# Performance work log

Measured on AMD Instinct MI355X. Metric: run time of the kernel, lower is better.

The kernel has to match this reference:

```python
import jax, jax.numpy as jnp
import numpy as np

N_HEAD = 16
D_HEAD = 64
D_MODEL = 1024
SCALE = 1.0 / float(D_HEAD) ** 0.5
LN_EPS = 1e-5


def _rel_shift(x):
    # x: [b, n, i, j] -> Transformer-XL relative shift
    b, n, i, j = x.shape
    x = jnp.pad(x, ((0, 0), (0, 0), (0, 0), (1, 0)))  # zero-pad front of last dim
    x = x.reshape(b, n, j + 1, i)[:, :, 1:, :]
    return x.reshape(b, n, i, j)


def _layer_norm(x, g, b):
    mu = jnp.mean(x, axis=-1, keepdims=True)
    var = jnp.mean(jnp.square(x - mu), axis=-1, keepdims=True)
    return g * (x - mu) / jnp.sqrt(var + LN_EPS) + b


def setup_inputs() -> dict:
    key = jax.random.key(0)
    ks = jax.random.split(key, 8)
    qlen, bsz = 1024, 4
    w = jax.random.normal(ks[0], (qlen, bsz, D_MODEL), jnp.float32)
    r = jax.random.normal(ks[1], (qlen, D_MODEL), jnp.float32)
    r_w_bias = 0.02 * jax.random.normal(ks[2], (N_HEAD, D_HEAD), jnp.float32)
    r_r_bias = 0.02 * jax.random.normal(ks[3], (N_HEAD, D_HEAD), jnp.float32)
    attn_mask = jnp.triu(jnp.ones((qlen, qlen), bool), 1)  # causal, True = masked
    qkv_w = 0.02 * jax.random.normal(ks[4], (D_MODEL, 3 * N_HEAD * D_HEAD), jnp.float32)
    qkv_b = jnp.zeros((3 * N_HEAD * D_HEAD,), jnp.float32)
    rk_w = 0.02 * jax.random.normal(ks[5], (D_MODEL, N_HEAD * D_HEAD), jnp.float32)
    rk_b = jnp.zeros((N_HEAD * D_HEAD,), jnp.float32)
    o_w = 0.02 * jax.random.normal(ks[6], (N_HEAD * D_HEAD, D_MODEL), jnp.float32)
    o_b = jnp.zeros((D_MODEL,), jnp.float32)
    ln_g = jnp.ones((D_MODEL,), jnp.float32)
    ln_b = jnp.zeros((D_MODEL,), jnp.float32)
    return {"w": w, "r": r, "r_w_bias": r_w_bias, "r_r_bias": r_r_bias,
            "qkv_w": qkv_w, "qkv_b": qkv_b, "rk_w": rk_w, "rk_b": rk_b,
            "o_w": o_w, "o_b": o_b, "ln_g": ln_g, "ln_b": ln_b,
            "attn_mask": attn_mask}


def reference(w, r, r_w_bias, r_r_bias, qkv_w, qkv_b, rk_w, rk_b, o_w, o_b, ln_g, ln_b, attn_mask):
    qlen, bsz, _ = w.shape
    # post-lnorm path (pre_lnorm=False)
    heads = w @ qkv_w + qkv_b                       # [q, b, 3*H*D]
    q, k, v = jnp.split(heads, 3, axis=-1)
    q = q.reshape(qlen, bsz, N_HEAD, D_HEAD)
    k = k.reshape(qlen, bsz, N_HEAD, D_HEAD)
    v = v.reshape(qlen, bsz, N_HEAD, D_HEAD)
    rk = (r @ rk_w + rk_b).reshape(-1, N_HEAD, D_HEAD)  # [rlen, H, D]
    AC = jnp.einsum('ibnd,jbnd->bnij', q + r_w_bias, k)
    BD = _rel_shift(jnp.einsum('ibnd,jnd->bnij', q + r_r_bias, rk))
    score = SCALE * (AC + BD)                       # [b, H, q, k]
    score = jnp.where(attn_mask[None, None, :, :], -jnp.inf, score)
    prob = jax.nn.softmax(score, axis=-1)
    vec = jnp.einsum('bnij,jbnd->ibnd', prob, v).reshape(qlen, bsz, N_HEAD * D_HEAD)
    attn_out = vec @ o_w + o_b
    return _layer_norm(w + attn_out, ln_g, ln_b)
```

## Files before the change

kernel.cpp:

```cpp
#include <hip/hip_runtime.h>
#include <math.h>

#define QL 1024
#define BSZ 4
#define NH 16
#define DH 64
#define DM 1024
#define SCALE_F 0.125f

typedef __attribute__((ext_vector_type(8))) short bf16x8;
typedef __attribute__((ext_vector_type(4))) float f32x4;

__device__ __forceinline__ unsigned short f2bf(float f) {
  union { float f; unsigned int u; } c; c.f = f;
  unsigned int u = c.u;
  u += 0x7FFFu + ((u >> 16) & 1u);
  return (unsigned short)(u >> 16);
}
__device__ __forceinline__ float bf2f(unsigned short u) {
  union { unsigned int i; float f; } c; c.i = ((unsigned int)u) << 16;
  return c.f;
}
__device__ __forceinline__ float2 bfp2f(const unsigned short* p) {
  unsigned int u = *(const unsigned int*)p;
  union { unsigned int u; float f; } lo, hi;
  lo.u = (u & 0xFFFFu) << 16;
  hi.u = u & 0xFFFF0000u;
  return make_float2(lo.f, hi.f);
}

__device__ __forceinline__ void ld_lds16(const unsigned short* g, unsigned short* l) {
  __builtin_amdgcn_global_load_lds(
      (const __attribute__((address_space(1))) unsigned int*)g,
      (__attribute__((address_space(3))) unsigned int*)l, 16, 0, 0);
}

__device__ __forceinline__ bf16x8 frag64(const unsigned short* lds, int n, int s) {
  return *(const bf16x8*)(lds + n * 64 + ((s ^ (n & 7)) * 8));
}

__global__ __launch_bounds__(256) void prep_kernel(
    const float* __restrict__ w, const float* __restrict__ r,
    const float* __restrict__ qkv_w, const float* __restrict__ rk_w,
    const float* __restrict__ o_w,
    unsigned short* __restrict__ wb, unsigned short* __restrict__ rb,
    unsigned short* __restrict__ qkv_wt, unsigned short* __restrict__ rk_wt,
    unsigned short* __restrict__ o_wt) {
  __shared__ __align__(16) unsigned short t[64][72];
  const int bid = blockIdx.x, tid = threadIdx.x;
  if (bid < 2560) {
    const float* in = (bid < 2048) ? w : r;
    unsigned short* out = (bid < 2048) ? wb : rb;
    int idx = ((bid < 2048) ? bid : (bid - 2048)) * 256 + tid;
    float4 a = *(const float4*)(in + (size_t)idx * 8);
    float4 b = *(const float4*)(in + (size_t)idx * 8 + 4);
    unsigned short o[8] = {f2bf(a.x), f2bf(a.y), f2bf(a.z), f2bf(a.w),
                           f2bf(b.x), f2bf(b.y), f2bf(b.z), f2bf(b.w)};
    *(uint4*)(out + (size_t)idx * 8) = *(const uint4*)o;
    return;
  }
  const float* in; unsigned short* out; int N, n0, k0;
  if (bid < 3328) {
    int l = bid - 2560; in = qkv_w; out = qkv_wt; N = 3072;
    n0 = (l % 48) * 64; k0 = (l / 48) * 64;
  } else if (bid < 3584) {
    int l = bid - 3328; in = rk_w; out = rk_wt; N = 1024;
    n0 = (l & 15) * 64; k0 = (l >> 4) * 64;
  } else {
    int l = bid - 3584; in = o_w; out = o_wt; N = 1024;
    n0 = (l & 15) * 64; k0 = (l >> 4) * 64;
  }
  for (int f = tid; f < 1024; f += 256) {
    int rr = f >> 4, c4 = (f & 15) * 4;
    float4 v = *(const float4*)(in + (size_t)(k0 + rr) * N + n0 + c4);
    t[c4 + 0][rr] = f2bf(v.x); t[c4 + 1][rr] = f2bf(v.y);
    t[c4 + 2][rr] = f2bf(v.z); t[c4 + 3][rr] = f2bf(v.w);
  }
  __syncthreads();
  for (int f = tid; f < 512; f += 256) {
    int rr = f >> 3, seg = (f & 7) * 8;
    *(uint4*)(out + (size_t)(n0 + rr) * 1024 + k0 + seg) = *(const uint4*)&t[rr][seg];
  }
}

__global__ __launch_bounds__(256) void drk_kernel(const unsigned short* __restrict__ rkb,
                                                  const float* __restrict__ rwb,
                                                  const float* __restrict__ rrb,
                                                  float* __restrict__ drk) {
  int idx = blockIdx.x * 256 + threadIdx.x;
  int h = idx >> 10;
  const unsigned short* rp = rkb + (size_t)idx * DH;
  float s = 0.f;
  for (int d = 0; d < DH; d += 2) {
    float2 rv = bfp2f(rp + d);
    s += rv.x * (rrb[h * DH + d] - rwb[h * DH + d]) +
         rv.y * (rrb[h * DH + d + 1] - rwb[h * DH + d + 1]);
  }
  drk[idx] = s;
}

template <int MODE>
__global__ __launch_bounds__(256) void gemm_bt(
    const unsigned short* __restrict__ A, const unsigned short* __restrict__ BT,
    const float* __restrict__ bias, float* __restrict__ Cf,
    unsigned short* __restrict__ O0, unsigned short* __restrict__ O1,
    unsigned short* __restrict__ O2, int M, int N, int K) {
  __shared__ __align__(16) unsigned short As[2 * 128 * 32];
  __shared__ __align__(16) unsigned short Bs[2 * 128 * 32];
  const int tid = threadIdx.x;
  const int w = tid >> 6, lane = tid & 63;
  const int quad = lane >> 4, l15 = lane & 15;
  const int wr = w >> 1, wc = w & 1;
  const int bm = blockIdx.y * 128, bn = blockIdx.x * 128;
  const int r_ = lane >> 2, sg = lane & 3;
  const int gs = sg ^ (r_ & 3);
  f32x4 acc[4][4] = {};

  auto stage = [&](int bf, int k0) {
#pragma unroll
    for (int i = 0; i < 2; ++i) {
      int row = (w * 2 + i) * 16 + r_;
      ld_lds16(A + (size_t)(bm + row) * K + k0 + gs * 8, As + bf * 4096 + (w * 2 + i) * 512);
      ld_lds16(BT + (size_t)(bn + row) * K + k0 + gs * 8, Bs + bf * 4096 + (w * 2 + i) * 512);
    }
  };

  int buf = 0;
  stage(0, 0);
  for (int k0 = 0; k0 < K; k0 += 32) {
    __syncthreads();
    if (k0 + 32 < K) stage(buf ^ 1, k0 + 32);
    const unsigned short* Al = As + buf * 4096;
    const unsigned short* Bl = Bs + buf * 4096;
    const int sa = quad ^ (l15 & 3);
    bf16x8 af[4], bf[4];
#pragma unroll
    for (int rt = 0; rt < 4; ++rt)
      af[rt] = *(const bf16x8*)&Al[(wr * 64 + rt * 16 + l15) * 32 + sa * 8];
#pragma unroll
    for (int nt = 0; nt < 4; ++nt)
      bf[nt] = *(const bf16x8*)&Bl[(wc * 64 + nt * 16 + l15) * 32 + sa * 8];
#pragma unroll
    for (int rt = 0; rt < 4; ++rt)
#pragma unroll
      for (int nt = 0; nt < 4; ++nt)
        acc[rt][nt] = __builtin_amdgcn_mfma_f32_16x16x32_bf16(af[rt], bf[nt], acc[rt][nt], 0, 0, 0);
    buf ^= 1;
  }

#pragma unroll
  for (int rt = 0; rt < 4; ++rt)
#pragma unroll
    for (int nt = 0; nt < 4; ++nt) {
      int gc = bn + wc * 64 + nt * 16 + l15;
      float bv = bias[gc];
#pragma unroll
      for (int reg = 0; reg < 4; ++reg) {
        int gr = bm + wr * 64 + rt * 16 + quad * 4 + reg;
        float val = acc[rt][nt][reg] + bv;
        if (MODE == 0) {
          int part = gc >> 10, h = (gc >> 6) & 15, d = gc & 63;
          int i = gr >> 2, b = gr & 3;
          if (part == 0)
            O0[((size_t)((b * NH + h) * QL + i)) * DH + d] = f2bf(val);
          else if (part == 1)
            O1[((size_t)((b * NH + h) * QL + i)) * DH + d] = f2bf(val);
          else
            O2[((size_t)((b * NH + h) * DH + d)) * QL + i] = f2bf(val);
        } else if (MODE == 1) {
          int h = gc >> 6, d = gc & 63;
          O0[((size_t)(h * QL + gr)) * DH + d] = f2bf(val);
        } else {
          Cf[(size_t)gr * N + gc] = val;
        }
      }
    }
}

__global__ __launch_bounds__(256, 4) void attn_kernel(
    const unsigned short* __restrict__ qbf, const unsigned short* __restrict__ kbf,
    const unsigned short* __restrict__ vtb, const unsigned short* __restrict__ rkb,
    const float* __restrict__ drk, const float* __restrict__ rwb,
    unsigned short* __restrict__ vecb) {
  __shared__ __align__(16) unsigned short ks[2 * 4096];
  __shared__ __align__(16) unsigned short vt[2 * 4096];
  __shared__ __align__(16) unsigned short bandps[4096];

  const int tid = threadIdx.x;
  const int w = tid >> 6, lane = tid & 63;
  const int quad = lane >> 4, l15 = lane & 15;
  const int bh = blockIdx.x, b = bh >> 4, h = bh & 15;
  const int i0 = (15 - (int)blockIdx.y) * 64;
  const int tdiag = i0 >> 6;

  const unsigned short* kB0 = kbf + (size_t)bh * QL * DH;
  const unsigned short* vB0 = vtb + (size_t)bh * DH * QL;
  const unsigned short* rB0 = rkb + (size_t)h * QL * DH;
  const float* drkh = drk + h * QL;

  const int srow = lane >> 3, sseg = lane & 7;

  auto stage_tile = [&](const unsigned short* gbase, size_t rstride, unsigned short* lds) {
#pragma unroll
    for (int ii = 0; ii < 2; ++ii) {
      int r = ii * 32 + w * 8 + srow;
      int gseg = sseg ^ (r & 7);
      ld_lds16(gbase + (size_t)r * rstride + gseg * 8, lds + ii * 2048 + w * 512);
    }
  };

  bf16x8 qf[2];
  {
    int qrow = i0 + w * 16 + l15;
    const unsigned short* qp = qbf + ((size_t)bh * QL + qrow) * DH;
#pragma unroll
    for (int s = 0; s < 2; ++s) {
      int off = s * 32 + quad * 8;
      uint4 raw = *(const uint4*)(qp + off);
      const unsigned short* ru = (const unsigned short*)&raw;
      float4 wb0 = *(const float4*)(rwb + h * DH + off);
      float4 wb1 = *(const float4*)(rwb + h * DH + off + 4);
      union { bf16x8 v; unsigned short u[8]; } qc;
      qc.u[0] = f2bf(bf2f(ru[0]) + wb0.x); qc.u[1] = f2bf(bf2f(ru[1]) + wb0.y);
      qc.u[2] = f2bf(bf2f(ru[2]) + wb0.z); qc.u[3] = f2bf(bf2f(ru[3]) + wb0.w);
      qc.u[4] = f2bf(bf2f(ru[4]) + wb1.x); qc.u[5] = f2bf(bf2f(ru[5]) + wb1.y);
      qc.u[6] = f2bf(bf2f(ru[6]) + wb1.z); qc.u[7] = f2bf(bf2f(ru[7]) + wb1.w);
      qf[s] = qc.v;
    }
  }

  auto rel_frag = [&](int gb, f32x4& c, float& dv) {
    int gc = min(gb + l15, 1023);
    const unsigned short* rp = rB0 + (size_t)gc * DH;
    f32x4 a = {0.f, 0.f, 0.f, 0.f};
    a = __builtin_amdgcn_mfma_f32_16x16x32_bf16(qf[0], *(const bf16x8*)(rp + quad * 8), a, 0, 0, 0);
    a = __builtin_amdgcn_mfma_f32_16x16x32_bf16(qf[1], *(const bf16x8*)(rp + 32 + quad * 8), a, 0, 0, 0);
    c = a;
    dv = drkh[gc];
  };

  stage_tile(kB0, DH, ks);
  stage_tile(vB0, QL, vt);

  f32x4 racc[5];
  float drkv[5];
#pragma unroll
  for (int i = 0; i < 5; ++i) rel_frag(1008 - i0 - 16 * w + 16 * i, racc[i], drkv[i]);

  float mrow[4], lrow[4];
  f32x4 pv[4];
#pragma unroll
  for (int r = 0; r < 4; ++r) {
    mrow[r] = -1e30f; lrow[r] = 0.f;
    pv[r] = (f32x4){0.f, 0.f, 0.f, 0.f};
  }

  int buf = 0;
  for (int t = 0; t <= tdiag; ++t) {
    __syncthreads();
    if (t < tdiag) {
      int j1 = (t + 1) << 6;
      stage_tile(kB0 + (size_t)j1 * DH, DH, ks + (buf ^ 1) * 4096);
      stage_tile(vB0 + j1, QL, vt + (buf ^ 1) * 4096);
    }
    if (t > 0) {
#pragma unroll
      for (int i = 0; i < 4; ++i) { racc[i] = racc[i + 1]; drkv[i] = drkv[i + 1]; }
#pragma unroll
      for (int i = 1; i < 5; ++i)
        rel_frag(1008 - i0 + 64 * t - 16 * w + 16 * i, racc[i], drkv[i]);
    }
    const int j0 = t << 6;
    const bool diag = (t == tdiag);
    const unsigned short* ksl = ks + buf * 4096;
    const unsigned short* vtl = vt + buf * 4096;

    f32x4 sacc[4];
#pragma unroll
    for (int nt = 0; nt < 4; ++nt) {
      int n = nt * 16 + l15;
      f32x4 c = {0.f, 0.f, 0.f, 0.f};
      c = __builtin_amdgcn_mfma_f32_16x16x32_bf16(qf[0], frag64(ksl, n, quad), c, 0, 0, 0);
      c = __builtin_amdgcn_mfma_f32_16x16x32_bf16(qf[1], frag64(ksl, n, 4 + quad), c, 0, 0, 0);
      sacc[nt] = c;
    }

#pragma unroll
    for (int i = 0; i < 5; ++i) {
      float dv = drkv[i];
#pragma unroll
      for (int r = 0; r < 4; ++r) {
        int c = 16 * i + l15 + 4 * quad + r - 15;
        int il = w * 16 + quad * 4 + r;
        if (c >= 0 && c < 64)
          bandps[il * 64 + (c ^ ((il & 7) << 3))] = f2bf(racc[i][r] + dv);
      }
    }

#pragma unroll
    for (int r = 0; r < 4; ++r) {
      const int il = w * 16 + quad * 4 + r;
      const int sw = (il & 7) << 3;
      float sv[4], smax = -1e30f;
#pragma unroll
      for (int nt = 0; nt < 4; ++nt) {
        int jl = nt * 16 + l15;
        float s = (sacc[nt][r] + bf2f(bandps[il * 64 + (jl ^ sw)])) * SCALE_F;
        if (diag && jl > il) s = -1e30f;
        sv[nt] = s;
        smax = fmaxf(smax, s);
      }
      smax = fmaxf(smax, __shfl_xor(smax, 1));
      smax = fmaxf(smax, __shfl_xor(smax, 2));
      smax = fmaxf(smax, __shfl_xor(smax, 4));
      smax = fmaxf(smax, __shfl_xor(smax, 8));
      float mnew = fmaxf(mrow[r], smax);
      float alpha = __expf(mrow[r] - mnew);
      mrow[r] = mnew;
      float psum = 0.f;
#pragma unroll
      for (int nt = 0; nt < 4; ++nt) {
        float e = __expf(sv[nt] - mnew);
        bandps[il * 64 + ((nt * 16 + l15) ^ sw)] = f2bf(e);
        psum += e;
      }
      psum += __shfl_xor(psum, 1);
      psum += __shfl_xor(psum, 2);
      psum += __shfl_xor(psum, 4);
      psum += __shfl_xor(psum, 8);
      lrow[r] = lrow[r] * alpha + psum;
#pragma unroll
      for (int nt = 0; nt < 4; ++nt) pv[nt][r] *= alpha;
    }

    {
      const int ilr = w * 16 + l15;
      const int swr = ilr & 7;
      bf16x8 pf0 = *(const bf16x8*)&bandps[ilr * 64 + ((quad ^ swr) * 8)];
      bf16x8 pf1 = *(const bf16x8*)&bandps[ilr * 64 + (((4 + quad) ^ swr) * 8)];
#pragma unroll
      for (int nt = 0; nt < 4; ++nt) {
        int n = nt * 16 + l15;
        pv[nt] = __builtin_amdgcn_mfma_f32_16x16x32_bf16(pf0, frag64(vtl, n, quad), pv[nt], 0, 0, 0);
        pv[nt] = __builtin_amdgcn_mfma_f32_16x16x32_bf16(pf1, frag64(vtl, n, 4 + quad), pv[nt], 0, 0, 0);
      }
    }
    buf ^= 1;
  }

#pragma unroll
  for (int nt = 0; nt < 4; ++nt)
#pragma unroll
    for (int reg = 0; reg < 4; ++reg) {
      int il = w * 16 + quad * 4 + reg;
      int gi = i0 + il;
      int d = nt * 16 + l15;
      float val = pv[nt][reg] / lrow[reg];
      vecb[((size_t)(gi * BSZ + b)) * DM + h * DH + d] = f2bf(val);
    }
}

__global__ __launch_bounds__(256) void ln_kernel(
    const float* __restrict__ w, const float* __restrict__ attn,
    const float* __restrict__ g, const float* __restrict__ bta,
    float* __restrict__ out) {
  __shared__ float red[4];
  __shared__ float sval[2];
  const int row = blockIdx.x, tid = threadIdx.x;
  const float* wr = w + (size_t)row * DM;
  const float* ar = attn + (size_t)row * DM;
  float4 wv = *(const float4*)(wr + tid * 4);
  float4 av = *(const float4*)(ar + tid * 4);
  float x0 = wv.x + av.x, x1 = wv.y + av.y, x2 = wv.z + av.z, x3 = wv.w + av.w;
  float s = x0 + x1 + x2 + x3;
#pragma unroll
  for (int off = 32; off; off >>= 1) s += __shfl_down(s, off, 64);
  const int lane = tid & 63, wvi = tid >> 6;
  if (lane == 0) red[wvi] = s;
  __syncthreads();
  if (tid == 0) sval[0] = (red[0] + red[1] + red[2] + red[3]) * (1.0f / 1024.0f);
  __syncthreads();
  const float mu = sval[0];
  float d0 = x0 - mu, d1 = x1 - mu, d2 = x2 - mu, d3 = x3 - mu;
  float vs2 = d0 * d0 + d1 * d1 + d2 * d2 + d3 * d3;
#pragma unroll
  for (int off = 32; off; off >>= 1) vs2 += __shfl_down(vs2, off, 64);
  if (lane == 0) red[wvi] = vs2;
  __syncthreads();
  if (tid == 0)
    sval[1] = rsqrtf((red[0] + red[1] + red[2] + red[3]) * (1.0f / 1024.0f) + 1e-5f);
  __syncthreads();
  const float inv = sval[1];
  float4 gv = *(const float4*)(g + tid * 4);
  float4 bv = *(const float4*)(bta + tid * 4);
  float4 ov;
  ov.x = gv.x * d0 * inv + bv.x;
  ov.y = gv.y * d1 * inv + bv.y;
  ov.z = gv.z * d2 * inv + bv.z;
  ov.w = gv.w * d3 * inv + bv.w;
  *(float4*)(out + (size_t)row * DM + tid * 4) = ov;
}

extern "C" void kernel_launch(void* const* d_in, const int* in_sizes, int n_in,
                              void* d_out, int out_size, void* d_ws, size_t ws_size,
                              hipStream_t stream) {
  const float* w     = (const float*)d_in[0];
  const float* r     = (const float*)d_in[1];
  const float* rwb   = (const float*)d_in[2];
  const float* rrb   = (const float*)d_in[3];
  const float* qkv_w = (const float*)d_in[4];
  const float* qkv_b = (const float*)d_in[5];
  const float* rk_w  = (const float*)d_in[6];
  const float* rk_b  = (const float*)d_in[7];
  const float* o_w   = (const float*)d_in[8];
  const float* o_b   = (const float*)d_in[9];
  const float* ln_g  = (const float*)d_in[10];
  const float* ln_b  = (const float*)d_in[11];

  float* out = (float*)d_out;
  char* p = (char*)d_ws;
  unsigned short* wb     = (unsigned short*)p; p += (size_t)4096 * 1024 * 2;
  unsigned short* rb     = (unsigned short*)p; p += (size_t)1024 * 1024 * 2;
  unsigned short* qkv_wt = (unsigned short*)p; p += (size_t)3072 * 1024 * 2;
  unsigned short* rk_wt  = (unsigned short*)p; p += (size_t)1024 * 1024 * 2;
  unsigned short* o_wt   = (unsigned short*)p; p += (size_t)1024 * 1024 * 2;
  unsigned short* qbf    = (unsigned short*)p; p += (size_t)BSZ * NH * QL * DH * 2;
  unsigned short* kbf    = (unsigned short*)p; p += (size_t)BSZ * NH * QL * DH * 2;
  unsigned short* vtb    = (unsigned short*)p; p += (size_t)BSZ * NH * QL * DH * 2;
  unsigned short* rkbf   = (unsigned short*)p; p += (size_t)NH * QL * DH * 2;
  float*          drk    = (float*)p;          p += (size_t)NH * QL * 4;
  unsigned short* vecb   = (unsigned short*)p; p += (size_t)4096 * 1024 * 2;
  float*          attnf  = (float*)p;          p += (size_t)4096 * 1024 * 4;

  prep_kernel<<<3840, 256, 0, stream>>>(w, r, qkv_w, rk_w, o_w,
                                        wb, rb, qkv_wt, rk_wt, o_wt);
  gemm_bt<0><<<dim3(24, 32), 256, 0, stream>>>(wb, qkv_wt, qkv_b, nullptr,
                                               qbf, kbf, vtb, 4096, 3072, 1024);
  gemm_bt<1><<<dim3(8, 8), 256, 0, stream>>>(rb, rk_wt, rk_b, nullptr,
                                             rkbf, nullptr, nullptr, 1024, 1024, 1024);
  drk_kernel<<<64, 256, 0, stream>>>(rkbf, rwb, rrb, drk);
  attn_kernel<<<dim3(64, 16), 256, 0, stream>>>(qbf, kbf, vtb, rkbf, drk, rwb, vecb);
  gemm_bt<2><<<dim3(8, 32), 256, 0, stream>>>(vecb, o_wt, o_b, attnf,
                                              nullptr, nullptr, nullptr, 4096, 1024, 1024);
  ln_kernel<<<4096, 256, 0, stream>>>(w, attnf, ln_g, ln_b, out);
}
```

Before: 313.2 us.

## Merge QKV and rel-key GEMMs with drk fusion, pair causal attention tiles per block

The QKV and relative-key projections now run in one 832-block, 512-thread GEMM launch. The rel-key epilogue computes drk with shuffle reductions and atomicAdd after a memset, which removes the separate drk kernel. The output GEMM also moves to 512 threads with 4x2 wave tiling. The attention kernel processes two query tiles per block (y and 15-y) so every block does the same amount of causal work, sharing K/V staging across both, and the grid is halved. The cost is more registers per attention thread, with the occupancy hint dropped, plus atomic traffic for drk.

Measured after the change: 307.9 us. About the same (-1.7%).

```diff
diff --git a/kernel.cpp b/kernel.cpp
--- a/kernel.cpp
+++ b/kernel.cpp
@@ -83,115 +83,197 @@
   }
 }
 
-__global__ __launch_bounds__(256) void drk_kernel(const unsigned short* __restrict__ rkb,
-                                                  const float* __restrict__ rwb,
-                                                  const float* __restrict__ rrb,
-                                                  float* __restrict__ drk) {
-  int idx = blockIdx.x * 256 + threadIdx.x;
-  int h = idx >> 10;
-  const unsigned short* rp = rkb + (size_t)idx * DH;
-  float s = 0.f;
-  for (int d = 0; d < DH; d += 2) {
-    float2 rv = bfp2f(rp + d);
-    s += rv.x * (rrb[h * DH + d] - rwb[h * DH + d]) +
-         rv.y * (rrb[h * DH + d + 1] - rwb[h * DH + d + 1]);
-  }
-  drk[idx] = s;
-}
-
-template <int MODE>
-__global__ __launch_bounds__(256) void gemm_bt(
+__global__ __launch_bounds__(512) void gemm12(
+    const unsigned short* __restrict__ wb, const unsigned short* __restrict__ rb,
+    const unsigned short* __restrict__ qkv_wt, const unsigned short* __restrict__ rk_wt,
+    const float* __restrict__ qkv_b, const float* __restrict__ rk_b,
+    const float* __restrict__ rwb, const float* __restrict__ rrb,
+    unsigned short* __restrict__ qbf, unsigned short* __restrict__ kbf,
+    unsigned short* __restrict__ vtb, unsigned short* __restrict__ rkbf,
+    float* __restrict__ drk) {
+  __shared__ __align__(16) unsigned short As[2 * 4096];
+  __shared__ __align__(16) unsigned short Bs[2 * 4096];
+  const int bid = blockIdx.x, tid = threadIdx.x;
+  const int w = tid >> 6, lane = tid & 63;
+  const int quad = lane >> 4, l15 = lane & 15;
+  const int wr = w >> 2, wc = w & 3;
+  const bool job0 = bid < 768;
+  const unsigned short *A, *BT;
+  const float* bias;
+  int bm, bn;
+  if (job0) {
+    A = wb; BT = qkv_wt; bias = qkv_b;
+    bn = (bid % 24) * 128; bm = (bid / 24) * 128;
+  } else {
+    int l = bid - 768;
+    A = rb; BT = rk_wt; bias = rk_b;
+    bn = (l & 7) * 128; bm = (l >> 3) * 128;
+  }
+  const int srow = w * 16 + (lane >> 2);
+  const int sseg = (lane & 3) ^ ((lane >> 2) & 3);
+  f32x4 acc[4][2] = {};
+
+  auto stage = [&](int bf, int k0) {
+    ld_lds16(A + (size_t)(bm + srow) * 1024 + k0 + sseg * 8, As + bf * 4096 + w * 512);
+    ld_lds16(BT + (size_t)(bn + srow) * 1024 + k0 + sseg * 8, Bs + bf * 4096 + w * 512);
+  };
+
+  int buf = 0;
+  stage(0, 0);
+  for (int k0 = 0; k0 < 1024; k0 += 32) {
+    __syncthreads();
+    if (k0 + 32 < 1024) stage(buf ^ 1, k0 + 32);
+    const unsigned short* Al = As + buf * 4096;
+    const unsigned short* Bl = Bs + buf * 4096;
+    const int sa = quad ^ (l15 & 3);
+    bf16x8 af[4], bfr[2];
+#pragma unroll
+    for (int rt = 0; rt < 4; ++rt)
+      af[rt] = *(const bf16x8*)&Al[(wr * 64 + rt * 16 + l15) * 32 + sa * 8];
+#pragma unroll
+    for (int nt = 0; nt < 2; ++nt)
+      bfr[nt] = *(const bf16x8*)&Bl[(wc * 32 + nt * 16 + l15) * 32 + sa * 8];
+#pragma unroll
+    for (int rt = 0; rt < 4; ++rt)
+#pragma unroll
+      for (int nt = 0; nt < 2; ++nt)
+        acc[rt][nt] = __builtin_amdgcn_mfma_f32_16x16x32_bf16(af[rt], bfr[nt], acc[rt][nt], 0, 0, 0);
+    buf ^= 1;
+  }
+
+  if (job0) {
+#pragma unroll
+    for (int rt = 0; rt < 4; ++rt)
+#pragma unroll
+      for (int nt = 0; nt < 2; ++nt) {
+        int gc = bn + wc * 32 + nt * 16 + l15;
+        float bv = bias[gc];
+        int part = gc >> 10, h = (gc >> 6) & 15, d = gc & 63;
+#pragma unroll
+        for (int reg = 0; reg < 4; ++reg) {
+          int gr = bm + wr * 64 + rt * 16 + quad * 4 + reg;
+          float val = acc[rt][nt][reg] + bv;
+          int i = gr >> 2, b = gr & 3;
+          if (part == 0)
+            qbf[((size_t)((b * NH + h) * QL + i)) * DH + d] = f2bf(val);
+          else if (part == 1)
+            kbf[((size_t)((b * NH + h) * QL + i)) * DH + d] = f2bf(val);
+          else
+            vtb[((size_t)((b * NH + h) * DH + d)) * QL + i] = f2bf(val);
+        }
+      }
+  } else {
+    const int h = (bn + wc * 32) >> 6;
+    float df[2];
+#pragma unroll
+    for (int nt = 0; nt < 2; ++nt) {
+      int dd = (wc & 1) * 32 + nt * 16 + l15;
+      df[nt] = rrb[h * DH + dd] - rwb[h * DH + dd];
+    }
+#pragma unroll
+    for (int rt = 0; rt < 4; ++rt) {
+      float s[4] = {0.f, 0.f, 0.f, 0.f};
+#pragma unroll
+      for (int nt = 0; nt < 2; ++nt) {
+        int gc = bn + wc * 32 + nt * 16 + l15;
+        float bv = bias[gc];
+        int d = gc & 63;
+#pragma unroll
+        for (int reg = 0; reg < 4; ++reg) {
+          int gr = bm + wr * 64 + rt * 16 + quad * 4 + reg;
+          float val = acc[rt][nt][reg] + bv;
+          rkbf[((size_t)(h * QL + gr)) * DH + d] = f2bf(val);
+          s[reg] += val * df[nt];
+        }
+      }
+#pragma unroll
+      for (int reg = 0; reg < 4; ++reg) {
+        float v = s[reg];
+        v += __shfl_xor(v, 1);
+        v += __shfl_xor(v, 2);
+        v += __shfl_xor(v, 4);
+        v += __shfl_xor(v, 8);
+        if (l15 == 0) {
+          int j = bm + wr * 64 + rt * 16 + quad * 4 + reg;
+          atomicAdd(&drk[h * QL + j], v);
+        }
+      }
+    }
+  }
+}
+
+__global__ __launch_bounds__(512) void gemm_o(
     const unsigned short* __restrict__ A, const unsigned short* __restrict__ BT,
-    const float* __restrict__ bias, float* __restrict__ Cf,
-    unsigned short* __restrict__ O0, unsigned short* __restrict__ O1,
-    unsigned short* __restrict__ O2, int M, int N, int K) {
-  __shared__ __align__(16) unsigned short As[2 * 128 * 32];
-  __shared__ __align__(16) unsigned short Bs[2 * 128 * 32];
+    const float* __restrict__ bias, float* __restrict__ Cf) {
+  __shared__ __align__(16) unsigned short As[2 * 4096];
+  __shared__ __align__(16) unsigned short Bs[2 * 4096];
   const int tid = threadIdx.x;
   const int w = tid >> 6, lane = tid & 63;
   const int quad = lane >> 4, l15 = lane & 15;
-  const int wr = w >> 1, wc = w & 1;
+  const int wr = w >> 2, wc = w & 3;
   const int bm = blockIdx.y * 128, bn = blockIdx.x * 128;
-  const int r_ = lane >> 2, sg = lane & 3;
-  const int gs = sg ^ (r_ & 3);
-  f32x4 acc[4][4] = {};
+  const int srow = w * 16 + (lane >> 2);
+  const int sseg = (lane & 3) ^ ((lane >> 2) & 3);
+  f32x4 acc[4][2] = {};
 
   auto stage = [&](int bf, int k0) {
-#pragma unroll
-    for (int i = 0; i < 2; ++i) {
-      int row = (w * 2 + i) * 16 + r_;
-      ld_lds16(A + (size_t)(bm + row) * K + k0 + gs * 8, As + bf * 4096 + (w * 2 + i) * 512);
-      ld_lds16(BT + (size_t)(bn + row) * K + k0 + gs * 8, Bs + bf * 4096 + (w * 2 + i) * 512);
-    }
+    ld_lds16(A + (size_t)(bm + srow) * 1024 + k0 + sseg * 8, As + bf * 4096 + w * 512);
+    ld_lds16(BT + (size_t)(bn + srow) * 1024 + k0 + sseg * 8, Bs + bf * 4096 + w * 512);
   };
 
   int buf = 0;
   stage(0, 0);
-  for (int k0 = 0; k0 < K; k0 += 32) {
+  for (int k0 = 0; k0 < 1024; k0 += 32) {
     __syncthreads();
-    if (k0 + 32 < K) stage(buf ^ 1, k0 + 32);
+    if (k0 + 32 < 1024) stage(buf ^ 1, k0 + 32);
     const unsigned short* Al = As + buf * 4096;
     const unsigned short* Bl = Bs + buf * 4096;
     const int sa = quad ^ (l15 & 3);
-    bf16x8 af[4], bf[4];
+    bf16x8 af[4], bfr[2];
 #pragma unroll
     for (int rt = 0; rt < 4; ++rt)
       af[rt] = *(const bf16x8*)&Al[(wr * 64 + rt * 16 + l15) * 32 + sa * 8];
 #pragma unroll
-    for (int nt = 0; nt < 4; ++nt)
-      bf[nt] = *(const bf16x8*)&Bl[(wc * 64 + nt * 16 + l15) * 32 + sa * 8];
+    for (int nt = 0; nt < 2; ++nt)
+      bfr[nt] = *(const bf16x8*)&Bl[(wc * 32 + nt * 16 + l15) * 32 + sa * 8];
 #pragma unroll
     for (int rt = 0; rt < 4; ++rt)
 #pragma unroll
-      for (int nt = 0; nt < 4; ++nt)
-        acc[rt][nt] = __builtin_amdgcn_mfma_f32_16x16x32_bf16(af[rt], bf[nt], acc[rt][nt], 0, 0, 0);
+      for (int nt = 0; nt < 2; ++nt)
+        acc[rt][nt] = __builtin_amdgcn_mfma_f32_16x16x32_bf16(af[rt], bfr[nt], acc[rt][nt], 0, 0, 0);
     buf ^= 1;
   }
 
 #pragma unroll
   for (int rt = 0; rt < 4; ++rt)
 #pragma unroll
-    for (int nt = 0; nt < 4; ++nt) {
-      int gc = bn + wc * 64 + nt * 16 + l15;
+    for (int nt = 0; nt < 2; ++nt) {
+      int gc = bn + wc * 32 + nt * 16 + l15;
       float bv = bias[gc];
 #pragma unroll
       for (int reg = 0; reg < 4; ++reg) {
         int gr = bm + wr * 64 + rt * 16 + quad * 4 + reg;
-        float val = acc[rt][nt][reg] + bv;
-        if (MODE == 0) {
-          int part = gc >> 10, h = (gc >> 6) & 15, d = gc & 63;
-          int i = gr >> 2, b = gr & 3;
-          if (part == 0)
-            O0[((size_t)((b * NH + h) * QL + i)) * DH + d] = f2bf(val);
-          else if (part == 1)
-            O1[((size_t)((b * NH + h) * QL + i)) * DH + d] = f2bf(val);
-          else
-            O2[((size_t)((b * NH + h) * DH + d)) * QL + i] = f2bf(val);
-        } else if (MODE == 1) {
-          int h = gc >> 6, d = gc & 63;
-          O0[((size_t)(h * QL + gr)) * DH + d] = f2bf(val);
-        } else {
-          Cf[(size_t)gr * N + gc] = val;
-        }
-      }
-    }
-}
-
-__global__ __launch_bounds__(256, 4) void attn_kernel(
+        Cf[(size_t)gr * DM + gc] = acc[rt][nt][reg] + bv;
+      }
+    }
+}
+
+__global__ __launch_bounds__(256) void attn_kernel(
     const unsigned short* __restrict__ qbf, const unsigned short* __restrict__ kbf,
     const unsigned short* __restrict__ vtb, const unsigned short* __restrict__ rkb,
     const float* __restrict__ drk, const float* __restrict__ rwb,
     unsigned short* __restrict__ vecb) {
   __shared__ __align__(16) unsigned short ks[2 * 4096];
   __shared__ __align__(16) unsigned short vt[2 * 4096];
-  __shared__ __align__(16) unsigned short bandps[4096];
+  __shared__ __align__(16) unsigned short band[2][4096];
 
   const int tid = threadIdx.x;
   const int w = tid >> 6, lane = tid & 63;
   const int quad = lane >> 4, l15 = lane & 15;
   const int bh = blockIdx.x, b = bh >> 4, h = bh & 15;
-  const int i0 = (15 - (int)blockIdx.y) * 64;
-  const int tdiag = i0 >> 6;
+  const int yA = blockIdx.y;
+  const int i0A = yA * 64, i0B = (15 - yA) * 64;
+  const int tA = yA, tB = 15 - yA;
 
   const unsigned short* kB0 = kbf + (size_t)bh * QL * DH;
   const unsigned short* vB0 = vtb + (size_t)bh * DH * QL;
@@ -199,7 +281,6 @@
   const float* drkh = drk + h * QL;
 
   const int srow = lane >> 3, sseg = lane & 7;
-
   auto stage_tile = [&](const unsigned short* gbase, size_t rstride, unsigned short* lds) {
 #pragma unroll
     for (int ii = 0; ii < 2; ++ii) {
@@ -209,8 +290,7 @@
     }
   };
 
-  bf16x8 qf[2];
-  {
+  auto load_q = [&](int i0, bf16x8* qf) {
     int qrow = i0 + w * 16 + l15;
     const unsigned short* qp = qbf + ((size_t)bh * QL + qrow) * DH;
 #pragma unroll
@@ -227,10 +307,13 @@
       qc.u[6] = f2bf(bf2f(ru[6]) + wb1.z); qc.u[7] = f2bf(bf2f(ru[7]) + wb1.w);
       qf[s] = qc.v;
     }
-  }
-
-  auto rel_frag = [&](int gb, f32x4& c, float& dv) {
-    int gc = min(gb + l15, 1023);
+  };
+  bf16x8 qfA[2], qfB[2];
+  load_q(i0A, qfA);
+  load_q(i0B, qfB);
+
+  auto rel_frag = [&](int gb, const bf16x8* qf, f32x4& c, float& dv) {
+    int gc = min(gb + l15, QL - 1);
     const unsigned short* rp = rB0 + (size_t)gc * DH;
     f32x4 a = {0.f, 0.f, 0.f, 0.f};
     a = __builtin_amdgcn_mfma_f32_16x16x32_bf16(qf[0], *(const bf16x8*)(rp + quad * 8), a, 0, 0, 0);
@@ -242,39 +325,25 @@
   stage_tile(kB0, DH, ks);
   stage_tile(vB0, QL, vt);
 
-  f32x4 racc[5];
-  float drkv[5];
-#pragma unroll
-  for (int i = 0; i < 5; ++i) rel_frag(1008 - i0 - 16 * w + 16 * i, racc[i], drkv[i]);
-
-  float mrow[4], lrow[4];
-  f32x4 pv[4];
+  f32x4 raccA[5], raccB[5];
+  float dvA[5], dvB[5];
+#pragma unroll
+  for (int i = 0; i < 5; ++i) {
+    rel_frag(1008 - i0A - 16 * w + 16 * i, qfA, raccA[i], dvA[i]);
+    rel_frag(1008 - i0B - 16 * w + 16 * i, qfB, raccB[i], dvB[i]);
+  }
+
+  float mA[4], lA[4], mB[4], lB[4];
+  f32x4 pvA[4], pvB[4];
 #pragma unroll
   for (int r = 0; r < 4; ++r) {
-    mrow[r] = -1e30f; lrow[r] = 0.f;
-    pv[r] = (f32x4){0.f, 0.f, 0.f, 0.f};
-  }
-
-  int buf = 0;
-  for (int t = 0; t <= tdiag; ++t) {
-    __syncthreads();
-    if (t < tdiag) {
-      int j1 = (t + 1) << 6;
-      stage_tile(kB0 + (size_t)j1 * DH, DH, ks + (buf ^ 1) * 4096);
-      stage_tile(vB0 + j1, QL, vt + (buf ^ 1) * 4096);
-    }
-    if (t > 0) {
-#pragma unroll
-      for (int i = 0; i < 4; ++i) { racc[i] = racc[i + 1]; drkv[i] = drkv[i + 1]; }
-#pragma unroll
-      for (int i = 1; i < 5; ++i)
-        rel_frag(1008 - i0 + 64 * t - 16 * w + 16 * i, racc[i], drkv[i]);
-    }
-    const int j0 = t << 6;
-    const bool diag = (t == tdiag);
-    const unsigned short* ksl = ks + buf * 4096;
-    const unsigned short* vtl = vt + buf * 4096;
-
+    mA[r] = mB[r] = -1e30f; lA[r] = lB[r] = 0.f;
+    pvA[r] = pvB[r] = (f32x4){0.f, 0.f, 0.f, 0.f};
+  }
+
+  auto do_stream = [&](const bf16x8* qf, f32x4* racc, float* dv, float* mrow, float* lrow,
+                       f32x4* pv, bool diag, const unsigned short* ksl,
+                       const unsigned short* vtl, unsigned short* bandS) {
     f32x4 sacc[4];
 #pragma unroll
     for (int nt = 0; nt < 4; ++nt) {
@@ -284,19 +353,17 @@
       c = __builtin_amdgcn_mfma_f32_16x16x32_bf16(qf[1], frag64(ksl, n, 4 + quad), c, 0, 0, 0);
       sacc[nt] = c;
     }
-
 #pragma unroll
     for (int i = 0; i < 5; ++i) {
-      float dv = drkv[i];
+      float dvv = dv[i];
 #pragma unroll
       for (int r = 0; r < 4; ++r) {
         int c = 16 * i + l15 + 4 * quad + r - 15;
         int il = w * 16 + quad * 4 + r;
         if (c >= 0 && c < 64)
-          bandps[il * 64 + (c ^ ((il & 7) << 3))] = f2bf(racc[i][r] + dv);
-      }
-    }
-
+          bandS[il * 64 + (c ^ ((il & 7) << 3))] = f2bf(racc[i][r] + dvv);
+      }
+    }
 #pragma unroll
     for (int r = 0; r < 4; ++r) {
       const int il = w * 16 + quad * 4 + r;
@@ -305,7 +372,7 @@
 #pragma unroll
       for (int nt = 0; nt < 4; ++nt) {
         int jl = nt * 16 + l15;
-        float s = (sacc[nt][r] + bf2f(bandps[il * 64 + (jl ^ sw)])) * SCALE_F;
+        float s = (sacc[nt][r] + bf2f(bandS[il * 64 + (jl ^ sw)])) * SCALE_F;
         if (diag && jl > il) s = -1e30f;
         sv[nt] = s;
         smax = fmaxf(smax, s);
@@ -321,7 +388,7 @@
 #pragma unroll
       for (int nt = 0; nt < 4; ++nt) {
         float e = __expf(sv[nt] - mnew);
-        bandps[il * 64 + ((nt * 16 + l15) ^ sw)] = f2bf(e);
+        bandS[il * 64 + ((nt * 16 + l15) ^ sw)] = f2bf(e);
         psum += e;
       }
       psum += __shfl_xor(psum, 1);
@@ -332,12 +399,11 @@
 #pragma unroll
       for (int nt = 0; nt < 4; ++nt) pv[nt][r] *= alpha;
     }
-
     {
       const int ilr = w * 16 + l15;
       const int swr = ilr & 7;
-      bf16x8 pf0 = *(const bf16x8*)&bandps[ilr * 64 + ((quad ^ swr) * 8)];
-      bf16x8 pf1 = *(const bf16x8*)&bandps[ilr * 64 + (((4 + quad) ^ swr) * 8)];
+      bf16x8 pf0 = *(const bf16x8*)&bandS[ilr * 64 + ((quad ^ swr) * 8)];
+      bf16x8 pf1 = *(const bf16x8*)&bandS[ilr * 64 + (((4 + quad) ^ swr) * 8)];
 #pragma unroll
       for (int nt = 0; nt < 4; ++nt) {
         int n = nt * 16 + l15;
@@ -345,6 +411,36 @@
         pv[nt] = __builtin_amdgcn_mfma_f32_16x16x32_bf16(pf1, frag64(vtl, n, 4 + quad), pv[nt], 0, 0, 0);
       }
     }
+  };
+
+  int buf = 0;
+  for (int t = 0; t <= tB; ++t) {
+    __syncthreads();
+    if (t < tB) {
+      int j1 = (t + 1) << 6;
+      stage_tile(kB0 + (size_t)j1 * DH, DH, ks + (buf ^ 1) * 4096);
+      stage_tile(vB0 + j1, QL, vt + (buf ^ 1) * 4096);
+    }
+    const unsigned short* ksl = ks + buf * 4096;
+    const unsigned short* vtl = vt + buf * 4096;
+    const bool actA = (t <= tA);
+
+    if (t > 0) {
+      raccB[0] = raccB[4]; dvB[0] = dvB[4];
+      const int GB = 1008 - i0B + 64 * t - 16 * w;
+#pragma unroll
+      for (int i = 1; i < 5; ++i) rel_frag(GB + 16 * i, qfB, raccB[i], dvB[i]);
+      if (actA) {
+        raccA[0] = raccA[4]; dvA[0] = dvA[4];
+        const int GA = 1008 - i0A + 64 * t - 16 * w;
+#pragma unroll
+        for (int i = 1; i < 5; ++i) rel_frag(GA + 16 * i, qfA, raccA[i], dvA[i]);
+      }
+    }
+
+    do_stream(qfB, raccB, dvB, mB, lB, pvB, t == tB, ksl, vtl, band[1]);
+    if (actA)
+      do_stream(qfA, raccA, dvA, mA, lA, pvA, t == tA, ksl, vtl, band[0]);
     buf ^= 1;
   }
 
@@ -353,10 +449,9 @@
 #pragma unroll
     for (int reg = 0; reg < 4; ++reg) {
       int il = w * 16 + quad * 4 + reg;
-      int gi = i0 + il;
       int d = nt * 16 + l15;
-      float val = pv[nt][reg] / lrow[reg];
-      vecb[((size_t)(gi * BSZ + b)) * DM + h * DH + d] = f2bf(val);
+      vecb[((size_t)((i0A + il) * BSZ + b)) * DM + h * DH + d] = f2bf(pvA[nt][reg] / lA[reg]);
+      vecb[((size_t)((i0B + il) * BSZ + b)) * DM + h * DH + d] = f2bf(pvB[nt][reg] / lB[reg]);
     }
 }
 
@@ -434,13 +529,10 @@
 
   prep_kernel<<<3840, 256, 0, stream>>>(w, r, qkv_w, rk_w, o_w,
                                         wb, rb, qkv_wt, rk_wt, o_wt);
-  gemm_bt<0><<<dim3(24, 32), 256, 0, stream>>>(wb, qkv_wt, qkv_b, nullptr,
-                                               qbf, kbf, vtb, 4096, 3072, 1024);
-  gemm_bt<1><<<dim3(8, 8), 256, 0, stream>>>(rb, rk_wt, rk_b, nullptr,
-                                             rkbf, nullptr, nullptr, 1024, 1024, 1024);
-  drk_kernel<<<64, 256, 0, stream>>>(rkbf, rwb, rrb, drk);
-  attn_kernel<<<dim3(64, 16), 256, 0, stream>>>(qbf, kbf, vtb, rkbf, drk, rwb, vecb);
-  gemm_bt<2><<<dim3(8, 32), 256, 0, stream>>>(vecb, o_wt, o_b, attnf,
-                                              nullptr, nullptr, nullptr, 4096, 1024, 1024);
+  hipMemsetAsync(drk, 0, (size_t)NH * QL * 4, stream);
+  gemm12<<<832, 512, 0, stream>>>(wb, rb, qkv_wt, rk_wt, qkv_b, rk_b, rwb, rrb,
+                                  qbf, kbf, vtb, rkbf, drk);
+  attn_kernel<<<dim3(64, 8), 256, 0, stream>>>(qbf, kbf, vtb, rkbf, drk, rwb, vecb);
+  gemm_o<<<dim3(8, 32), 512, 0, stream>>>(vecb, o_wt, o_b, attnf);
   ln_kernel<<<4096, 256, 0, stream>>>(w, attnf, ln_g, ln_b, out);
 }
```
